# Performance work log

Measured on AMD Instinct MI355X. Metric: run time of the kernel, lower is better.

Reference implementation:

```python
import jax, jax.numpy as jnp
from jax import lax
import numpy as np

RPN_BBOX_STD_DEV = np.array([0.1, 0.1, 0.2, 0.2], dtype=np.float32)
PRE_NMS_LIMIT = 2048      # anchors kept before NMS (sorted by score)
NUM_PROPOSAL = 1000       # post-NMS proposal count (init kwarg num_proposal)
NMS_THRESHOLD = 0.7       # init kwarg nms_threshold


def setup_inputs() -> dict:
    key = jax.random.key(0)
    k1, k2, k3, k4, k5, k6 = jax.random.split(key, 6)
    B, N = 4, 1_000_000
    rpn_probs = jax.random.uniform(k1, (B, N, 2), dtype=jnp.float32)
    rpn_bbox = jax.random.normal(k2, (B, N, 4), dtype=jnp.float32)
    # well-formed normalized anchors (y1, x1, y2, x2)
    cy = jax.random.uniform(k3, (B, N), dtype=jnp.float32)
    cx = jax.random.uniform(k4, (B, N), dtype=jnp.float32)
    h = jax.random.uniform(k5, (B, N), dtype=jnp.float32) * 0.25 + 0.05
    w = jax.random.uniform(k6, (B, N), dtype=jnp.float32) * 0.25 + 0.05
    anchors = jnp.stack([cy - 0.5 * h, cx - 0.5 * w, cy + 0.5 * h, cx + 0.5 * w], axis=-1)
    return {"rpn_probs": rpn_probs, "rpn_bbox": rpn_bbox, "anchors": anchors}


def apply_box_deltas(boxes, deltas):
    # boxes: (..., 4) as (y1, x1, y2, x2); deltas: (dy, dx, log(dh), log(dw))
    h = boxes[..., 2] - boxes[..., 0]
    w = boxes[..., 3] - boxes[..., 1]
    cy = boxes[..., 0] + 0.5 * h + deltas[..., 0] * h
    cx = boxes[..., 1] + 0.5 * w + deltas[..., 1] * w
    h = h * jnp.exp(deltas[..., 2])
    w = w * jnp.exp(deltas[..., 3])
    return jnp.stack([cy - 0.5 * h, cx - 0.5 * w, cy + 0.5 * h, cx + 0.5 * w], axis=-1)


def pairwise_iou(boxes):
    # boxes: (P, 4) -> (P, P)
    y1, x1, y2, x2 = boxes[:, 0], boxes[:, 1], boxes[:, 2], boxes[:, 3]
    area = (y2 - y1) * (x2 - x1)
    ih = jnp.maximum(jnp.minimum(y2[:, None], y2[None, :]) - jnp.maximum(y1[:, None], y1[None, :]), 0.0)
    iw = jnp.maximum(jnp.minimum(x2[:, None], x2[None, :]) - jnp.maximum(x1[:, None], x1[None, :]), 0.0)
    inter = ih * iw
    union = area[:, None] + area[None, :] - inter
    return inter / (union + 1e-8)


def nms_single(boxes):
    # boxes (P, 4) sorted by score desc; greedy NMS then pad/clip to NUM_PROPOSAL
    P = boxes.shape[0]
    iou = pairwise_iou(boxes)
    idx = jnp.arange(P)

    def body(keep, i):
        suppress = keep[i] & (iou[i] > NMS_THRESHOLD) & (idx > i)
        return keep & ~suppress, None

    keep, _ = lax.scan(body, jnp.ones((P,), jnp.bool_), idx)
    rank = jnp.cumsum(keep) - 1                      # position among kept boxes
    valid = keep & (rank < NUM_PROPOSAL)
    pos = jnp.where(valid, rank, NUM_PROPOSAL)       # overflow row dropped below
    out = jnp.zeros((NUM_PROPOSAL + 1, 4), boxes.dtype).at[pos].set(
        jnp.where(valid[:, None], boxes, 0.0))
    return out[:NUM_PROPOSAL]


def reference(rpn_probs, rpn_bbox, anchors):
    scores = rpn_probs[:, :, 1]                                  # foreground prob (B, N)
    deltas = rpn_bbox * jnp.asarray(RPN_BBOX_STD_DEV)
    _, ix = lax.top_k(scores, PRE_NMS_LIMIT)                     # (B, P)
    deltas_top = jnp.take_along_axis(deltas, ix[..., None], axis=1)
    anchors_top = jnp.take_along_axis(anchors, ix[..., None], axis=1)
    boxes = apply_box_deltas(anchors_top, deltas_top)            # (B, P, 4)
    boxes = jnp.clip(boxes, 0.0, 1.0)                            # clip to [0,1] window
    proposals = jax.vmap(nms_single)(boxes)                      # (B, NUM_PROPOSAL, 4)
    return proposals
```

## Files before the change

kernel.cpp:

```cpp
#include <hip/hip_runtime.h>

#define B_ 4
#define N_ 1000000
#define K_ 2048
#define P_ 1000
#define CAP_ 8192
#define THR_ 0.7f
#define NF4_ 500000
#define META_STRIDE 32
#define TILE_ 512
#define NCH_ (CAP_ / TILE_)
#define SRANK 128

#define OFF_META 0
#define OFF_CAND 1024
#define OFF_BOX  263168
#define OFF_MASK 394240

__device__ __forceinline__ unsigned fkey(float f) {
  unsigned u = __float_as_uint(f);
  return (u & 0x80000000u) ? ~u : (u | 0x80000000u);
}

__device__ __forceinline__ unsigned long long readlane64(unsigned long long v, int l) {
  unsigned lo = (unsigned)__builtin_amdgcn_readlane((int)(unsigned)(v & 0xffffffffull), l);
  unsigned hi = (unsigned)__builtin_amdgcn_readlane((int)(unsigned)(v >> 32), l);
  return ((unsigned long long)hi << 32) | (unsigned long long)lo;
}

#define PIN16(k) asm volatile("" : "+v"(k[0]), "+v"(k[1]), "+v"(k[2]), "+v"(k[3]), \
                                   "+v"(k[4]), "+v"(k[5]), "+v"(k[6]), "+v"(k[7]), \
                                   "+v"(k[8]), "+v"(k[9]), "+v"(k[10]), "+v"(k[11]), \
                                   "+v"(k[12]), "+v"(k[13]), "+v"(k[14]), "+v"(k[15]))

__global__ void __launch_bounds__(1024) sample_select_kernel(const float4* __restrict__ probs4,
                                                             unsigned* __restrict__ meta) {
  int b = blockIdx.x, t = threadIdx.x;
  __shared__ unsigned h32[8192];
  __shared__ unsigned suf[1024];
  __shared__ int tg_s;
  __shared__ unsigned above_s;
  if (t == 0) meta[b * META_STRIDE + 1] = 0u;
  for (int i = t; i < 8192; i += 1024) h32[i] = 0u;
  __syncthreads();
  const float4* p4 = probs4 + (size_t)b * NF4_;
#pragma unroll
  for (int it = 0; it < 16; ++it) {
    int i = it * 1024 + t;
    int c = i >> 8, pos = i & 255;
    float4 v = p4[c * 7800 + pos];
    int b0 = (int)(fkey(v.y) >> 16) - 0x8000;
    int b1 = (int)(fkey(v.w) >> 16) - 0x8000;
    b0 = b0 < 0 ? 0 : (b0 > 16383 ? 16383 : b0);
    b1 = b1 < 0 ? 0 : (b1 > 16383 ? 16383 : b1);
    atomicAdd(&h32[b0 >> 1], 1u << ((b0 & 1) << 4));
    atomicAdd(&h32[b1 >> 1], 1u << ((b1 & 1) << 4));
  }
  __syncthreads();
  {
    unsigned s = 0;
    const unsigned* p = &h32[t * 8];
#pragma unroll
    for (int i = 0; i < 8; ++i) { unsigned x = p[i]; s += (x & 0xFFFFu) + (x >> 16); }
    suf[t] = s;
  }
  __syncthreads();
  for (int off = 1; off < 1024; off <<= 1) {
    unsigned add = (t + off < 1024) ? suf[t + off] : 0u;
    __syncthreads();
    suf[t] += add;
    __syncthreads();
  }
  unsigned nxt = (t < 1023) ? suf[t + 1] : 0u;
  if (suf[t] >= SRANK && (t == 1023 || nxt < SRANK)) { tg_s = t; above_s = nxt; }
  __syncthreads();
  if (t == 0) {
    int tg = tg_s;
    unsigned run = above_s;
    int cb = tg * 16;
    for (int i = 15; i >= 0; --i) {
      unsigned x = h32[tg * 8 + (i >> 1)];
      unsigned cnt = (i & 1) ? (x >> 16) : (x & 0xFFFFu);
      run += cnt;
      if (run >= SRANK) { cb = tg * 16 + i; break; }
    }
    meta[b * META_STRIDE + 0] = (unsigned)(cb + 0x8000);
  }
}

__global__ void __launch_bounds__(256) compact_kernel(const float4* __restrict__ probs4,
                                                      unsigned* __restrict__ meta,
                                                      uint2* __restrict__ cand) {
  int b = blockIdx.y;
  __shared__ unsigned lcnt, gbase_s;
  __shared__ uint2 buf[4096];
  if (threadIdx.x == 0) lcnt = 0u;
  __syncthreads();
  unsigned cb = meta[b * META_STRIDE + 0];
  const float4* p4 = probs4 + (size_t)b * NF4_;
  int base = blockIdx.x * 2048;
  int lane = threadIdx.x & 63;
  float4 v[8];
#pragma unroll
  for (int c = 0; c < 8; ++c) {
    int i4 = base + c * 256 + threadIdx.x;
    v[c] = (i4 < NF4_) ? p4[i4] : make_float4(0.f, 0.f, 0.f, 0.f);
  }
  unsigned k[16];
#pragma unroll
  for (int c = 0; c < 8; ++c) { k[2 * c] = fkey(v[c].y); k[2 * c + 1] = fkey(v[c].w); }
  PIN16(k);
#pragma unroll
  for (int c = 0; c < 8; ++c) {
#pragma unroll
    for (int s = 0; s < 2; ++s) {
      int i4 = base + c * 256 + threadIdx.x;
      unsigned key = k[2 * c + s];
      bool pass = (i4 < NF4_) && ((key >> 16) >= cb);
      unsigned long long m = __ballot(pass);
      if (m) {
        int leader = __ffsll(m) - 1;
        unsigned wbase = 0;
        if (lane == leader) wbase = atomicAdd(&lcnt, (unsigned)__popcll(m));
        wbase = __shfl(wbase, leader, 64);
        if (pass) {
          unsigned pos = wbase + (unsigned)__popcll(m & ((1ull << lane) - 1ull));
          buf[pos] = make_uint2(key, (unsigned)(2 * i4 + s));
        }
      }
    }
  }
  __syncthreads();
  unsigned cnt = lcnt;
  if (threadIdx.x == 0) gbase_s = atomicAdd(&meta[b * META_STRIDE + 1], cnt);
  __syncthreads();
  unsigned gbase = gbase_s;
  for (unsigned i = threadIdx.x; i < cnt; i += 256) {
    unsigned pos = gbase + i;
    if (pos < CAP_) cand[(size_t)b * CAP_ + pos] = buf[i];
  }
}

__global__ void __launch_bounds__(256) rank_kernel(const uint2* __restrict__ cand,
                                                   const unsigned* __restrict__ meta,
                                                   unsigned* __restrict__ partial) {
  int b = blockIdx.z;
  unsigned M = meta[b * META_STRIDE + 1];
  if (M > CAP_) M = CAP_;
  unsigned tb = blockIdx.y * TILE_;
  if (tb >= M) return;
  if ((unsigned)(blockIdx.x * 256) >= M) return;
  __shared__ __align__(16) uint2 tile[TILE_];
  unsigned n = M - tb;
  if (n > TILE_) n = TILE_;
  for (unsigned t = threadIdx.x; t < n; t += 256) tile[t] = cand[(size_t)b * CAP_ + tb + t];
  int ci = blockIdx.x * 256 + threadIdx.x;
  bool act = ci < (int)M;
  uint2 me = make_uint2(0u, 0u);
  if (act) me = cand[(size_t)b * CAP_ + ci];
  unsigned long long my = ((unsigned long long)me.x << 32) | (unsigned long long)(unsigned)(~me.y);
  __syncthreads();
  if (act) {
    unsigned rank = 0;
    unsigned n2 = n >> 1;
    const uint4* t4 = (const uint4*)tile;
    for (unsigned j = 0; j < n2; ++j) {
      uint4 v = t4[j];
      unsigned long long c0 = ((unsigned long long)v.x << 32) | (unsigned long long)(unsigned)(~v.y);
      unsigned long long c1 = ((unsigned long long)v.z << 32) | (unsigned long long)(unsigned)(~v.w);
      rank += (unsigned)(c0 > my) + (unsigned)(c1 > my);
    }
    if (n & 1) {
      uint2 v = tile[n - 1];
      unsigned long long c0 = ((unsigned long long)v.x << 32) | (unsigned long long)(unsigned)(~v.y);
      rank += (unsigned)(c0 > my);
    }
    partial[((size_t)b * NCH_ + blockIdx.y) * CAP_ + ci] = rank;
  }
}

__global__ void __launch_bounds__(256) scatter_kernel(const uint2* __restrict__ cand,
                                                      const unsigned* __restrict__ meta,
                                                      const unsigned* __restrict__ partial,
                                                      const float4* __restrict__ bbox,
                                                      const float4* __restrict__ anch,
                                                      float4* __restrict__ boxes) {
  int b = blockIdx.y;
  unsigned M = meta[b * META_STRIDE + 1];
  if (M > CAP_) M = CAP_;
  unsigned ci = blockIdx.x * 256 + threadIdx.x;
  if (ci >= M) return;
  unsigned nch = (M + TILE_ - 1) / TILE_;
  const unsigned* pp = partial + (size_t)b * NCH_ * CAP_ + ci;
  unsigned rank = 0;
  for (unsigned c = 0; c < nch; ++c) rank += pp[(size_t)c * CAP_];
  if (rank >= K_) return;
  unsigned idx = cand[(size_t)b * CAP_ + ci].y;
  size_t base = (size_t)b * N_ + idx;
  float4 a = anch[base];
  float4 d = bbox[base];
  float d0 = d.x * 0.1f, d1 = d.y * 0.1f, d2 = d.z * 0.2f, d3 = d.w * 0.2f;
  float h = a.z - a.x, w = a.w - a.y;
  float cy = (a.x + 0.5f * h) + d0 * h;
  float cx = (a.y + 0.5f * w) + d1 * w;
  float h2 = h * expf(d2);
  float w2 = w * expf(d3);
  float y1 = cy - 0.5f * h2, x1 = cx - 0.5f * w2;
  float y2 = cy + 0.5f * h2, x2 = cx + 0.5f * w2;
  y1 = fminf(fmaxf(y1, 0.f), 1.f);
  x1 = fminf(fmaxf(x1, 0.f), 1.f);
  y2 = fminf(fmaxf(y2, 0.f), 1.f);
  x2 = fminf(fmaxf(x2, 0.f), 1.f);
  boxes[(b << 11) + rank] = make_float4(y1, x1, y2, x2);
}

__global__ void mask_kernel(const float4* __restrict__ boxes, unsigned long long* __restrict__ mask) {
  int wid = blockIdx.x * 4 + (threadIdx.x >> 6);
  int lane = threadIdx.x & 63;
  int b = wid >> 12;
  int rb = (wid >> 5) & 127;
  int jb = wid & 31;
  if (jb < (rb >> 2)) return;
  int j = (jb << 6) + lane;
  float4 bj = boxes[(b << 11) + j];
  float areaJ = (bj.z - bj.x) * (bj.w - bj.y);
#pragma unroll
  for (int r = 0; r < 16; ++r) {
    int i = (rb << 4) + r;
    float4 bi = boxes[(b << 11) + i];
    float areaI = (bi.z - bi.x) * (bi.w - bi.y);
    float yA = fmaxf(bi.x, bj.x), xA = fmaxf(bi.y, bj.y);
    float yB = fminf(bi.z, bj.z), xB = fminf(bi.w, bj.w);
    float ih = fmaxf(yB - yA, 0.f), iw = fmaxf(xB - xA, 0.f);
    float inter = ih * iw;
    float uni = areaI + areaJ - inter;
    float iou = inter / (uni + 1e-8f);
    bool pred = (iou > THR_) && (j > i);
    unsigned long long bits = __ballot(pred);
    if (lane == 0) mask[((size_t)((b << 11) + i) << 5) + jb] = bits;
  }
}

__global__ void __launch_bounds__(64) nms_kernel(const unsigned long long* __restrict__ mask,
                                                 const float4* __restrict__ boxes,
                                                 float4* __restrict__ out) {
  int b = blockIdx.x;
  int lane = threadIdx.x;
  int w = lane & 31, half = lane >> 5;
  __shared__ unsigned long long rows[64][33];
  __shared__ unsigned long long keptm[32];
  __shared__ int pre[32];
  __shared__ short sel[P_];
  if (lane < 32) keptm[lane] = 0ull;
  for (int r = lane; r < P_; r += 64) sel[r] = -1;
  const unsigned long long* mbase = mask + (((size_t)(b << 11)) << 5);
  unsigned long long r0[32];
#pragma unroll
  for (int j = 0; j < 32; ++j) r0[j] = mbase[j * 64 + lane];
#pragma unroll
  for (int j = 0; j < 32; ++j) rows[2 * j + half][w] = r0[j];
  __syncthreads();
  unsigned long long rem = 0ull;
  int cnt = 0;
  for (int c = 0; c < 32; ++c) {
    bool pf = (c < 31) && (w > c);
    if (pf) {
      const unsigned long long* srcN = mbase + (((size_t)(c + 1)) << 11);
#pragma unroll
      for (int j = 0; j < 32; ++j) r0[j] = srcN[j * 64 + lane];
    }
    unsigned long long rin = rows[lane][c];
    unsigned long long cur = readlane64(rem, c);
    unsigned long long bm = __ballot(rin != 0ull) & ~cur;
    while (bm) {
      int k2 = __ffsll((long long)bm) - 1;
      bm &= bm - 1;
      if (!((cur >> k2) & 1ull)) {
        cur |= readlane64(rin, k2);
        bm &= ~cur;
      }
    }
    unsigned long long kept = ~cur;
    if (lane == 0) keptm[c] = kept;
    cnt += (int)__popcll(kept);
    if (cnt >= P_) break;
    if (w > c) {
      unsigned long long acc = 0ull;
#pragma unroll
      for (int k2 = 0; k2 < 32; ++k2) {
        int row = half * 32 + k2;
        acc |= rows[row][w] & (0ull - ((kept >> row) & 1ull));
      }
      acc |= __shfl_xor(acc, 32, 64);
      rem |= acc;
    }
    if (pf) {
#pragma unroll
      for (int j = 0; j < 32; ++j) rows[2 * j + half][w] = r0[j];
    }
    __syncthreads();
  }
  __syncthreads();
  if (lane == 0) {
    int run = 0;
    for (int c = 0; c < 32; ++c) { pre[c] = run; run += (int)__popcll(keptm[c]); }
  }
  __syncthreads();
  for (int i = lane; i < K_; i += 64) {
    int c = i >> 6, k2 = i & 63;
    unsigned long long km = keptm[c];
    if ((km >> k2) & 1ull) {
      int rank = pre[c] + (int)__popcll(km & ((1ull << k2) - 1ull));
      if (rank < P_) sel[rank] = (short)i;
    }
  }
  __syncthreads();
  for (int r = lane; r < P_; r += 64) {
    int i = sel[r];
    float4 v = make_float4(0.f, 0.f, 0.f, 0.f);
    if (i >= 0) v = boxes[(b << 11) + i];
    out[b * P_ + r] = v;
  }
}

extern "C" void kernel_launch(void* const* d_in, const int* in_sizes, int n_in,
                              void* d_out, int out_size, void* d_ws, size_t ws_size,
                              hipStream_t stream) {
  const float4* probs4 = (const float4*)d_in[0];
  const float4* bbox   = (const float4*)d_in[1];
  const float4* anch   = (const float4*)d_in[2];
  char* ws = (char*)d_ws;
  unsigned* meta = (unsigned*)(ws + OFF_META);
  uint2* cand = (uint2*)(ws + OFF_CAND);
  float4* boxes = (float4*)(ws + OFF_BOX);
  unsigned long long* mask = (unsigned long long*)(ws + OFF_MASK);
  unsigned* partial = (unsigned*)(ws + OFF_MASK);
  float4* out = (float4*)d_out;

  sample_select_kernel<<<B_, 1024, 0, stream>>>(probs4, meta);
  compact_kernel<<<dim3(245, B_), 256, 0, stream>>>(probs4, meta, cand);
  rank_kernel<<<dim3(CAP_ / 256, NCH_, B_), 256, 0, stream>>>(cand, meta, partial);
  scatter_kernel<<<dim3(CAP_ / 256, B_), 256, 0, stream>>>(cand, meta, partial, bbox, anch, boxes);
  mask_kernel<<<(B_ * 128 * 32) / 4, 256, 0, stream>>>(boxes, mask);
  nms_kernel<<<B_, 64, 0, stream>>>(mask, boxes, out);
}
```

Before: 230.8 us.

## Widen NMS to 256 threads with double-buffered mask rows and wave-shuffle scan

The sequential NMS kernel goes from one 64-lane wave to four waves. Mask row loads are spread across threads and double-buffered two chunks ahead, and the removal bits are accumulated in shared memory with atomicOr instead of per-lane registers. The histogram suffix scan in the select kernel changes from a 10-step shared-memory scan with barriers to wave shuffles plus a small cross-wave pass. The aim is to shorten the latency-bound serial NMS loop and cut barrier count, at the cost of extra shared-memory atomics and more barrier participants in each iteration.

```diff
diff --git a/kernel.cpp b/kernel.cpp
--- a/kernel.cpp
+++ b/kernel.cpp
@@ -36,8 +36,9 @@
 __global__ void __launch_bounds__(1024) sample_select_kernel(const float4* __restrict__ probs4,
                                                              unsigned* __restrict__ meta) {
   int b = blockIdx.x, t = threadIdx.x;
+  int wid = t >> 6, lane = t & 63;
   __shared__ unsigned h32[8192];
-  __shared__ unsigned suf[1024];
+  __shared__ unsigned waveTot[16], waveSuf[16];
   __shared__ int tg_s;
   __shared__ unsigned above_s;
   if (t == 0) meta[b * META_STRIDE + 1] = 0u;
@@ -57,22 +58,36 @@
     atomicAdd(&h32[b1 >> 1], 1u << ((b1 & 1) << 4));
   }
   __syncthreads();
+  unsigned cntT;
   {
     unsigned s = 0;
     const unsigned* p = &h32[t * 8];
 #pragma unroll
     for (int i = 0; i < 8; ++i) { unsigned x = p[i]; s += (x & 0xFFFFu) + (x >> 16); }
-    suf[t] = s;
-  }
-  __syncthreads();
-  for (int off = 1; off < 1024; off <<= 1) {
-    unsigned add = (t + off < 1024) ? suf[t + off] : 0u;
-    __syncthreads();
-    suf[t] += add;
-    __syncthreads();
-  }
-  unsigned nxt = (t < 1023) ? suf[t + 1] : 0u;
-  if (suf[t] >= SRANK && (t == 1023 || nxt < SRANK)) { tg_s = t; above_s = nxt; }
+    cntT = s;
+  }
+  unsigned sfx = cntT;
+#pragma unroll
+  for (int off = 1; off < 64; off <<= 1) {
+    unsigned v = __shfl_down(sfx, off, 64);
+    if (lane + off < 64) sfx += v;
+  }
+  if (lane == 0) waveTot[wid] = sfx;
+  __syncthreads();
+  if (t < 16) {
+    unsigned v = waveTot[t];
+    unsigned s2 = v;
+#pragma unroll
+    for (int off = 1; off < 16; off <<= 1) {
+      unsigned u = __shfl_down(s2, off, 64);
+      if (t + off < 16) s2 += u;
+    }
+    waveSuf[t] = s2 - v;
+  }
+  __syncthreads();
+  unsigned sufT = sfx + waveSuf[wid];
+  unsigned sufN = sufT - cntT;
+  if (sufT >= SRANK && (t == 1023 || sufN < SRANK)) { tg_s = t; above_s = sufN; }
   __syncthreads();
   if (t == 0) {
     int tg = tg_s;
@@ -241,36 +256,38 @@
   }
 }
 
-__global__ void __launch_bounds__(64) nms_kernel(const unsigned long long* __restrict__ mask,
-                                                 const float4* __restrict__ boxes,
-                                                 float4* __restrict__ out) {
+__global__ void __launch_bounds__(256) nms_kernel(const unsigned long long* __restrict__ mask,
+                                                  const float4* __restrict__ boxes,
+                                                  float4* __restrict__ out) {
   int b = blockIdx.x;
-  int lane = threadIdx.x;
-  int w = lane & 31, half = lane >> 5;
-  __shared__ unsigned long long rows[64][33];
+  int t = threadIdx.x;
+  int lane = t & 63;
+  int w = t & 31;
+  int rowb = t >> 5;
+  __shared__ unsigned long long rows[2][64][33];
+  __shared__ unsigned long long remS[32];
   __shared__ unsigned long long keptm[32];
   __shared__ int pre[32];
   __shared__ short sel[P_];
-  if (lane < 32) keptm[lane] = 0ull;
-  for (int r = lane; r < P_; r += 64) sel[r] = -1;
-  const unsigned long long* mbase = mask + (((size_t)(b << 11)) << 5);
-  unsigned long long r0[32];
-#pragma unroll
-  for (int j = 0; j < 32; ++j) r0[j] = mbase[j * 64 + lane];
-#pragma unroll
-  for (int j = 0; j < 32; ++j) rows[2 * j + half][w] = r0[j];
-  __syncthreads();
-  unsigned long long rem = 0ull;
+  if (t < 32) { remS[t] = 0ull; keptm[t] = 0ull; }
+  for (int r = t; r < P_; r += 256) sel[r] = -1;
+  const unsigned long long* mb = mask + (((size_t)(b << 11)) << 5);
+  unsigned long long rA[8], rB[8];
+#pragma unroll
+  for (int j = 0; j < 8; ++j) rA[j] = mb[j * 256 + t];
+#pragma unroll
+  for (int j = 0; j < 8; ++j) rows[0][8 * j + rowb][w] = rA[j];
+  {
+    bool ld = (w >= 1);
+#pragma unroll
+    for (int j = 0; j < 8; ++j) rB[j] = ld ? mb[2048 + j * 256 + t] : 0ull;
+  }
+  __syncthreads();
   int cnt = 0;
   for (int c = 0; c < 32; ++c) {
-    bool pf = (c < 31) && (w > c);
-    if (pf) {
-      const unsigned long long* srcN = mbase + (((size_t)(c + 1)) << 11);
-#pragma unroll
-      for (int j = 0; j < 32; ++j) r0[j] = srcN[j * 64 + lane];
-    }
-    unsigned long long rin = rows[lane][c];
-    unsigned long long cur = readlane64(rem, c);
+    int cb = c & 1;
+    unsigned long long rin = rows[cb][lane][c];
+    unsigned long long cur = remS[c];
     unsigned long long bm = __ballot(rin != 0ull) & ~cur;
     while (bm) {
       int k2 = __ffsll((long long)bm) - 1;
@@ -281,32 +298,53 @@
       }
     }
     unsigned long long kept = ~cur;
-    if (lane == 0) keptm[c] = kept;
+    if (t == 0) keptm[c] = kept;
     cnt += (int)__popcll(kept);
     if (cnt >= P_) break;
     if (w > c) {
       unsigned long long acc = 0ull;
 #pragma unroll
-      for (int k2 = 0; k2 < 32; ++k2) {
-        int row = half * 32 + k2;
-        acc |= rows[row][w] & (0ull - ((kept >> row) & 1ull));
-      }
-      acc |= __shfl_xor(acc, 32, 64);
-      rem |= acc;
-    }
-    if (pf) {
-#pragma unroll
-      for (int j = 0; j < 32; ++j) rows[2 * j + half][w] = r0[j];
+      for (int j = 0; j < 8; ++j) {
+        int row = 8 * j + rowb;
+        acc |= rows[cb][row][w] & (0ull - ((kept >> row) & 1ull));
+      }
+      if (acc) {
+        unsigned lo = (unsigned)acc, hi = (unsigned)(acc >> 32);
+        unsigned* rp = (unsigned*)&remS[w];
+        if (lo) atomicOr(rp, lo);
+        if (hi) atomicOr(rp + 1, hi);
+      }
+    }
+    if (c < 31) {
+      if (w >= c + 1) {
+        if (c & 1) {
+#pragma unroll
+          for (int j = 0; j < 8; ++j) rows[cb ^ 1][8 * j + rowb][w] = rA[j];
+        } else {
+#pragma unroll
+          for (int j = 0; j < 8; ++j) rows[cb ^ 1][8 * j + rowb][w] = rB[j];
+        }
+      }
+      if (c < 30 && w >= c + 2) {
+        const unsigned long long* src = mb + (size_t)(c + 2) * 2048;
+        if (c & 1) {
+#pragma unroll
+          for (int j = 0; j < 8; ++j) rB[j] = src[j * 256 + t];
+        } else {
+#pragma unroll
+          for (int j = 0; j < 8; ++j) rA[j] = src[j * 256 + t];
+        }
+      }
     }
     __syncthreads();
   }
   __syncthreads();
-  if (lane == 0) {
+  if (t == 0) {
     int run = 0;
     for (int c = 0; c < 32; ++c) { pre[c] = run; run += (int)__popcll(keptm[c]); }
   }
   __syncthreads();
-  for (int i = lane; i < K_; i += 64) {
+  for (int i = t; i < K_; i += 256) {
     int c = i >> 6, k2 = i & 63;
     unsigned long long km = keptm[c];
     if ((km >> k2) & 1ull) {
@@ -315,7 +353,7 @@
     }
   }
   __syncthreads();
-  for (int r = lane; r < P_; r += 64) {
+  for (int r = t; r < P_; r += 256) {
     int i = sel[r];
     float4 v = make_float4(0.f, 0.f, 0.f, 0.f);
     if (i >= 0) v = boxes[(b << 11) + i];
@@ -342,5 +380,5 @@
   rank_kernel<<<dim3(CAP_ / 256, NCH_, B_), 256, 0, stream>>>(cand, meta, partial);
   scatter_kernel<<<dim3(CAP_ / 256, B_), 256, 0, stream>>>(cand, meta, partial, bbox, anch, boxes);
   mask_kernel<<<(B_ * 128 * 32) / 4, 256, 0, stream>>>(boxes, mask);
-  nms_kernel<<<B_, 64, 0, stream>>>(mask, boxes, out);
-}
+  nms_kernel<<<B_, 256, 0, stream>>>(mask, boxes, out);
+}
```

Result: faster. 223.9 us (-3.0%).
